# Kernel tuning notes

Measured on AMD Instinct MI355X. Metric: run time of the kernel, lower is better.

Reference implementation:

```python
import jax, jax.numpy as jnp
import numpy as np

N, E, F_IN, H, C, G = 50000, 800000, 64, 4, 32, 64
N_CLS, N_EXP, HID = 8, 3, 128
NEG_SLOPE = 0.2  # PyG GATConv default negative_slope


def setup_inputs() -> dict:
    key = jax.random.key(0)
    ks = jax.random.split(key, 16)
    p = lambda k, s: jax.random.normal(k, s, dtype=jnp.float32) * 0.05
    return {
        "x": jax.random.normal(ks[0], (N, F_IN), dtype=jnp.float32),
        "edge_index": jax.random.randint(ks[1], (2, E), 0, N),
        "batch": jnp.sort(jax.random.randint(ks[2], (N,), 0, G)),
        "set_idx": 0,
        "enc_W1": p(ks[3], (F_IN, H * C)),
        "enc_as1": p(ks[4], (H, C)),
        "enc_ad1": p(ks[5], (H, C)),
        "enc_b1": jnp.zeros((H * C,), jnp.float32),
        "enc_W2": p(ks[6], (H * C, H * C)),
        "enc_as2": p(ks[7], (H, C)),
        "enc_ad2": p(ks[8], (H, C)),
        "enc_b2": jnp.zeros((H * C,), jnp.float32),
        "cls_W1": p(ks[9], (2 * H * C, HID)),
        "cls_b1": jnp.zeros((HID,), jnp.float32),
        "cls_Wo": p(ks[10], (HID, N_CLS)),
        "cls_bo": jnp.zeros((N_CLS,), jnp.float32),
        "dis_W1": p(ks[11], (2 * H * C, HID)),
        "dis_b1": jnp.zeros((HID,), jnp.float32),
        "dis_Wo": p(ks[12], (HID, N_EXP)),
        "dis_bo": jnp.zeros((N_EXP,), jnp.float32),
    }


def gat_conv(x, src, dst, W, att_src, att_dst, bias):
    """PyG GATConv (concat=True, self-loops already in src/dst)."""
    n = x.shape[0]
    h = (x @ W).reshape(n, H, C)                     # [N,H,C]
    a_src = (h * att_src).sum(-1)                    # [N,H]
    a_dst = (h * att_dst).sum(-1)                    # [N,H]
    e = jax.nn.leaky_relu(a_src[src] + a_dst[dst], NEG_SLOPE)  # [E,H]
    e_max = jax.ops.segment_max(e, dst, num_segments=n)
    ee = jnp.exp(e - e_max[dst])
    denom = jax.ops.segment_sum(ee, dst, num_segments=n)
    alpha = ee / (denom[dst] + 1e-16)                # softmax over in-edges
    msg = h[src] * alpha[:, :, None]                 # [E,H,C]
    out = jax.ops.segment_sum(msg, dst, num_segments=n).reshape(n, H * C)
    return out + bias


def mlp(x, W1, b1, Wo, bo):
    return jax.nn.relu(x @ W1 + b1) @ Wo + bo


def reference(x, edge_index, batch, set_idx,
              enc_W1, enc_as1, enc_ad1, enc_b1,
              enc_W2, enc_as2, enc_ad2, enc_b2,
              cls_W1, cls_b1, cls_Wo, cls_bo,
              dis_W1, dis_b1, dis_Wo, dis_bo):
    n = x.shape[0]
    loop = jnp.arange(n)
    src = jnp.concatenate([edge_index[0], loop])     # add self-loops
    dst = jnp.concatenate([edge_index[1], loop])
    h = jax.nn.relu(gat_conv(x, src, dst, enc_W1, enc_as1, enc_ad1, enc_b1))
    h = gat_conv(h, src, dst, enc_W2, enc_as2, enc_ad2, enc_b2)
    counts = jax.ops.segment_sum(jnp.ones((n,), h.dtype), batch, num_segments=G)
    x_mean = jax.ops.segment_sum(h, batch, num_segments=G) / jnp.maximum(counts, 1.0)[:, None]
    x_max = jax.ops.segment_max(h, batch, num_segments=G)
    feat = jnp.concatenate([x_mean, x_max], axis=1)  # [G, 256]
    feat = feat / jnp.maximum(jnp.linalg.norm(feat, axis=1, keepdims=True), 1e-12)
    label_pred = mlp(feat, cls_W1, cls_b1, cls_Wo, cls_bo)
    # grad_reverse is identity in the forward pass
    batch_pred = mlp(feat, dis_W1, dis_b1, dis_Wo, dis_bo)
    return (label_pred, batch_pred)
```

## Files before the change

### kernel.cpp

```cpp
#include <hip/hip_runtime.h>
#include <float.h>

#define HC 128
#define NH 4
#define PSLICES 8
#define BSHIFT 9
#define NBK 128
#define NBH 512

__device__ __forceinline__ float lrelu(float v){ return v > 0.f ? v : 0.2f*v; }

__device__ __forceinline__ unsigned short f2bf(float f){
  unsigned int u = __float_as_uint(f);
  unsigned int r = (u + 0x7fffu + ((u >> 16) & 1u)) >> 16;
  return (unsigned short)r;
}

__global__ void k_hist(const int* __restrict__ ei, int* __restrict__ gmat,
                       int E, int T, int chunk){
  __shared__ int h[NBK];
  int b = blockIdx.x, t = threadIdx.x;
  if (t < NBK) h[t] = 0;
  __syncthreads();
  int lo = b*chunk, hi = lo + chunk; if (hi > T) hi = T;
  for (int i = lo + t; i < hi; i += 256){
    int d = (i < E) ? ei[E + i] : (i - E);
    atomicAdd(&h[d >> BSHIFT], 1);
  }
  __syncthreads();
  if (t < NBK) gmat[(size_t)b*NBK + t] = h[t];
}

__global__ void k_colscan(int* __restrict__ gmat, int* __restrict__ coltot){
  __shared__ int part[256];
  int k = blockIdx.x, t = threadIdx.x;
  int v0 = gmat[(size_t)(2*t)*NBK + k];
  int v1 = gmat[(size_t)(2*t+1)*NBK + k];
  int s = v0 + v1;
  part[t] = s;
  __syncthreads();
  for (int off = 1; off < 256; off <<= 1){
    int v = (t >= off) ? part[t-off] : 0;
    __syncthreads();
    part[t] += v;
    __syncthreads();
  }
  int pre = part[t] - s;
  gmat[(size_t)(2*t)*NBK + k]   = pre;
  gmat[(size_t)(2*t+1)*NBK + k] = pre + v0;
  if (t == 255) coltot[k] = part[255];
}

__global__ void k_bstart(const int* __restrict__ coltot, int* __restrict__ bstart,
                         int* __restrict__ rowptrN){
  __shared__ int part[NBK];
  int t = threadIdx.x;
  int own = coltot[t];
  part[t] = own;
  __syncthreads();
  for (int off = 1; off < NBK; off <<= 1){
    int v = (t >= off) ? part[t-off] : 0;
    __syncthreads();
    part[t] += v;
    __syncthreads();
  }
  bstart[t] = part[t] - own;
  if (t == NBK-1){ bstart[NBK] = part[NBK-1]; *rowptrN = part[NBK-1]; }
}

__global__ void k_bucket(const int* __restrict__ ei, const int* __restrict__ gmat,
                         const int* __restrict__ bstart, int2* __restrict__ pairs,
                         int E, int T, int chunk){
  __shared__ int cnt[NBK];
  int b = blockIdx.x, t = threadIdx.x;
  if (t < NBK) cnt[t] = 0;
  __syncthreads();
  int lo = b*chunk, hi = lo + chunk; if (hi > T) hi = T;
  for (int i = lo + t; i < hi; i += 256){
    int s, d;
    if (i < E){ s = ei[i]; d = ei[E + i]; } else { s = d = i - E; }
    int k = d >> BSHIFT;
    int r = atomicAdd(&cnt[k], 1);
    int pos = bstart[k] + gmat[(size_t)b*NBK + k] + r;
    pairs[pos] = make_int2(d, s);
  }
}

__global__ void k_csr(const int2* __restrict__ pairs, const int* __restrict__ bstart,
                      int* __restrict__ rowptr, int* __restrict__ srcs, int N){
  __shared__ int deg[512];
  __shared__ int off[512];
  __shared__ int part[256];
  int k = blockIdx.x, t = threadIdx.x;
  int nlo = k << BSHIFT;
  int nhi = nlo + 512; if (nhi > N) nhi = N;
  int nn = nhi - nlo;
  int elo = bstart[k], ehi = bstart[k+1];
  deg[t] = 0; deg[t + 256] = 0;
  __syncthreads();
  for (int i = elo + t; i < ehi; i += 256) atomicAdd(&deg[pairs[i].x - nlo], 1);
  __syncthreads();
  int v0 = deg[2*t], v1 = deg[2*t+1];
  int s = v0 + v1;
  part[t] = s;
  __syncthreads();
  for (int o = 1; o < 256; o <<= 1){
    int v = (t >= o) ? part[t-o] : 0;
    __syncthreads();
    part[t] += v;
    __syncthreads();
  }
  int pre = part[t] - s;
  off[2*t] = pre; off[2*t+1] = pre + v0;
  __syncthreads();
  for (int j = t; j < nn; j += 256) rowptr[nlo + j] = elo + off[j];
  deg[t] = 0; deg[t + 256] = 0;
  __syncthreads();
  for (int i = elo + t; i < ehi; i += 256){
    int2 p = pairs[i];
    int dl = p.x - nlo;
    int r = atomicAdd(&deg[dl], 1);
    srcs[elo + off[dl] + r] = p.y;
  }
}

template<int K>
__global__ __launch_bounds__(256) void k_gemm_att(
    const float* __restrict__ X, const float* __restrict__ W,
    const float* __restrict__ as_, const float* __restrict__ ad_,
    unsigned short* __restrict__ Hb, float* __restrict__ asrc, float* __restrict__ adst,
    int n)
{
  __shared__ float Ws[64][64];
  __shared__ float Xs[64][68];
  int tid = threadIdx.x;
  int tx = tid & 15;
  int ty = tid >> 4;
  int row0 = blockIdx.x * 64;
  int cbase = blockIdx.y * 64;

  float4 acc[4];
  #pragma unroll
  for (int i = 0; i < 4; ++i) acc[i] = make_float4(0.f,0.f,0.f,0.f);

  for (int kc = 0; kc < K; kc += 64){
    #pragma unroll
    for (int p = 0; p < 4; ++p){
      int idx = tid + 256*p;
      int rr = idx >> 4, kk = (idx & 15) * 4;
      float4 w = *reinterpret_cast<const float4*>(W + (size_t)(kc + rr)*HC + cbase + kk);
      *reinterpret_cast<float4*>(&Ws[rr][kk]) = w;
    }
    #pragma unroll
    for (int p = 0; p < 4; ++p){
      int idx = tid + 256*p;
      int rr = idx >> 4, kk = (idx & 15) * 4;
      int g = row0 + rr;
      float4 v = make_float4(0.f,0.f,0.f,0.f);
      if (g < n) v = *reinterpret_cast<const float4*>(X + (size_t)g*K + kc + kk);
      *reinterpret_cast<float4*>(&Xs[rr][kk]) = v;
    }
    __syncthreads();
    #pragma unroll 4
    for (int k = 0; k < 64; ++k){
      float4 w = *reinterpret_cast<const float4*>(&Ws[k][tx*4]);
      #pragma unroll
      for (int i = 0; i < 4; ++i){
        float xv = Xs[ty + 16*i][k];
        acc[i].x += xv*w.x; acc[i].y += xv*w.y; acc[i].z += xv*w.z; acc[i].w += xv*w.w;
      }
    }
    __syncthreads();
  }

  int c0 = cbase + tx*4;
  int hd = c0 >> 5;
  float4 a4 = *reinterpret_cast<const float4*>(as_ + c0);
  float4 d4 = *reinterpret_cast<const float4*>(ad_ + c0);
  #pragma unroll
  for (int i = 0; i < 4; ++i){
    int row = row0 + ty + 16*i;
    float ps = acc[i].x*a4.x + acc[i].y*a4.y + acc[i].z*a4.z + acc[i].w*a4.w;
    float pd = acc[i].x*d4.x + acc[i].y*d4.y + acc[i].z*d4.z + acc[i].w*d4.w;
    ps += __shfl_down(ps, 4); pd += __shfl_down(pd, 4);
    ps += __shfl_down(ps, 2); pd += __shfl_down(pd, 2);
    ps += __shfl_down(ps, 1); pd += __shfl_down(pd, 1);
    if (row < n){
      uint2 pk;
      pk.x = (unsigned int)f2bf(acc[i].x) | ((unsigned int)f2bf(acc[i].y) << 16);
      pk.y = (unsigned int)f2bf(acc[i].z) | ((unsigned int)f2bf(acc[i].w) << 16);
      *reinterpret_cast<uint2*>(Hb + (size_t)row*HC + c0) = pk;
      if ((tx & 7) == 0){
        asrc[row*NH + hd] = ps;
        adst[row*NH + hd] = pd;
      }
    }
  }
}

__global__ void k_agg(const unsigned short* __restrict__ Xh, const float* __restrict__ asrc,
                      const float* __restrict__ adst, const int* __restrict__ rowptr,
                      const int* __restrict__ srcs, const float* __restrict__ bias,
                      float* __restrict__ out, int n, int do_relu)
{
  int lane = threadIdx.x & 63;
  int node = blockIdx.x*4 + (threadIdx.x >> 6);
  if (node >= n) return;
  int base = __builtin_amdgcn_readfirstlane(rowptr[node]);
  int deg  = __builtin_amdgcn_readfirstlane(rowptr[node+1]) - base;
  int hd = lane >> 4;
  float adh = adst[node*NH + hd];
  int c0 = lane*2;
  float accx = 0.f, accy = 0.f, wsum = 0.f;
  int j = 0;
  for (; j + 8 <= deg; j += 8){
    int s0 = __builtin_amdgcn_readfirstlane(srcs[base + j]);
    int s1 = __builtin_amdgcn_readfirstlane(srcs[base + j + 1]);
    int s2 = __builtin_amdgcn_readfirstlane(srcs[base + j + 2]);
    int s3 = __builtin_amdgcn_readfirstlane(srcs[base + j + 3]);
    int s4 = __builtin_amdgcn_readfirstlane(srcs[base + j + 4]);
    int s5 = __builtin_amdgcn_readfirstlane(srcs[base + j + 5]);
    int s6 = __builtin_amdgcn_readfirstlane(srcs[base + j + 6]);
    int s7 = __builtin_amdgcn_readfirstlane(srcs[base + j + 7]);
    unsigned int u0 = *reinterpret_cast<const unsigned int*>(Xh + (size_t)s0*HC + c0);
    unsigned int u1 = *reinterpret_cast<const unsigned int*>(Xh + (size_t)s1*HC + c0);
    unsigned int u2 = *reinterpret_cast<const unsigned int*>(Xh + (size_t)s2*HC + c0);
    unsigned int u3 = *reinterpret_cast<const unsigned int*>(Xh + (size_t)s3*HC + c0);
    unsigned int u4 = *reinterpret_cast<const unsigned int*>(Xh + (size_t)s4*HC + c0);
    unsigned int u5 = *reinterpret_cast<const unsigned int*>(Xh + (size_t)s5*HC + c0);
    unsigned int u6 = *reinterpret_cast<const unsigned int*>(Xh + (size_t)s6*HC + c0);
    unsigned int u7 = *reinterpret_cast<const unsigned int*>(Xh + (size_t)s7*HC + c0);
    float a0 = asrc[s0*NH + hd];
    float a1 = asrc[s1*NH + hd];
    float a2 = asrc[s2*NH + hd];
    float a3 = asrc[s3*NH + hd];
    float a4 = asrc[s4*NH + hd];
    float a5 = asrc[s5*NH + hd];
    float a6 = asrc[s6*NH + hd];
    float a7 = asrc[s7*NH + hd];
    float w0 = __expf(lrelu(a0 + adh));
    float w1 = __expf(lrelu(a1 + adh));
    float w2 = __expf(lrelu(a2 + adh));
    float w3 = __expf(lrelu(a3 + adh));
    float w4 = __expf(lrelu(a4 + adh));
    float w5 = __expf(lrelu(a5 + adh));
    float w6 = __expf(lrelu(a6 + adh));
    float w7 = __expf(lrelu(a7 + adh));
    wsum += ((w0 + w1) + (w2 + w3)) + ((w4 + w5) + (w6 + w7));
    accx += w0*__uint_as_float(u0 << 16) + w1*__uint_as_float(u1 << 16)
          + w2*__uint_as_float(u2 << 16) + w3*__uint_as_float(u3 << 16)
          + w4*__uint_as_float(u4 << 16) + w5*__uint_as_float(u5 << 16)
          + w6*__uint_as_float(u6 << 16) + w7*__uint_as_float(u7 << 16);
    accy += w0*__uint_as_float(u0 & 0xffff0000u) + w1*__uint_as_float(u1 & 0xffff0000u)
          + w2*__uint_as_float(u2 & 0xffff0000u) + w3*__uint_as_float(u3 & 0xffff0000u)
          + w4*__uint_as_float(u4 & 0xffff0000u) + w5*__uint_as_float(u5 & 0xffff0000u)
          + w6*__uint_as_float(u6 & 0xffff0000u) + w7*__uint_as_float(u7 & 0xffff0000u);
  }
  for (; j + 4 <= deg; j += 4){
    int s0 = __builtin_amdgcn_readfirstlane(srcs[base + j]);
    int s1 = __builtin_amdgcn_readfirstlane(srcs[base + j + 1]);
    int s2 = __builtin_amdgcn_readfirstlane(srcs[base + j + 2]);
    int s3 = __builtin_amdgcn_readfirstlane(srcs[base + j + 3]);
    unsigned int u0 = *reinterpret_cast<const unsigned int*>(Xh + (size_t)s0*HC + c0);
    unsigned int u1 = *reinterpret_cast<const unsigned int*>(Xh + (size_t)s1*HC + c0);
    unsigned int u2 = *reinterpret_cast<const unsigned int*>(Xh + (size_t)s2*HC + c0);
    unsigned int u3 = *reinterpret_cast<const unsigned int*>(Xh + (size_t)s3*HC + c0);
    float a0 = asrc[s0*NH + hd];
    float a1 = asrc[s1*NH + hd];
    float a2 = asrc[s2*NH + hd];
    float a3 = asrc[s3*NH + hd];
    float w0 = __expf(lrelu(a0 + adh));
    float w1 = __expf(lrelu(a1 + adh));
    float w2 = __expf(lrelu(a2 + adh));
    float w3 = __expf(lrelu(a3 + adh));
    wsum += (w0 + w1) + (w2 + w3);
    accx += w0*__uint_as_float(u0 << 16) + w1*__uint_as_float(u1 << 16)
          + w2*__uint_as_float(u2 << 16) + w3*__uint_as_float(u3 << 16);
    accy += w0*__uint_as_float(u0 & 0xffff0000u) + w1*__uint_as_float(u1 & 0xffff0000u)
          + w2*__uint_as_float(u2 & 0xffff0000u) + w3*__uint_as_float(u3 & 0xffff0000u);
  }
  for (; j < deg; ++j){
    int s = __builtin_amdgcn_readfirstlane(srcs[base + j]);
    unsigned int u = *reinterpret_cast<const unsigned int*>(Xh + (size_t)s*HC + c0);
    float w = __expf(lrelu(asrc[s*NH + hd] + adh));
    wsum += w;
    accx += w*__uint_as_float(u << 16);
    accy += w*__uint_as_float(u & 0xffff0000u);
  }
  float inv = 1.f / wsum;
  accx = accx*inv + bias[c0];
  accy = accy*inv + bias[c0+1];
  if (do_relu){ accx = fmaxf(accx, 0.f); accy = fmaxf(accy, 0.f); }
  *reinterpret_cast<float2*>(out + (size_t)node*HC + c0) = make_float2(accx, accy);
}

__global__ void k_bounds(const int* __restrict__ batch, int* __restrict__ start, int N, int G){
  for (int i = blockIdx.x*blockDim.x + threadIdx.x; i <= N; i += gridDim.x*blockDim.x){
    int b  = (i < N) ? batch[i]   : G;
    int bp = (i > 0) ? batch[i-1] : -1;
    for (int g = bp + 1; g <= b; ++g) if (g <= G) start[g] = i;
  }
}

__global__ void k_pool_partial(const float* __restrict__ h2, const int* __restrict__ start,
                               float* __restrict__ psum, float* __restrict__ pmax, int G){
  int g = blockIdx.x / PSLICES, s = blockIdx.x % PSLICES;
  int c = threadIdx.x;
  int st = start[g], en = start[g+1];
  float sm = 0.f, mx = -FLT_MAX;
  for (int i = st + s; i < en; i += PSLICES){
    float v = h2[(size_t)i*HC + c];
    sm += v; mx = fmaxf(mx, v);
  }
  psum[(g*PSLICES+s)*HC + c] = sm;
  pmax[(g*PSLICES+s)*HC + c] = mx;
}

__global__ void k_head(const float* __restrict__ psum, const float* __restrict__ pmax,
                       const int* __restrict__ start,
                       const float* __restrict__ cW1, const float* __restrict__ cb1,
                       const float* __restrict__ cWo, const float* __restrict__ cbo,
                       const float* __restrict__ dW1, const float* __restrict__ db1,
                       const float* __restrict__ dWo, const float* __restrict__ dbo,
                       float* __restrict__ out, int G){
  __shared__ float feat[256];
  __shared__ float hid[128];
  __shared__ float red[2];
  int g = blockIdx.x;
  int t = threadIdx.x;
  int cnt = start[g+1] - start[g];
  float sm = 0.f, mx = -FLT_MAX;
  for (int s = 0; s < PSLICES; ++s){
    sm += psum[(g*PSLICES+s)*HC + t];
    mx = fmaxf(mx, pmax[(g*PSLICES+s)*HC + t]);
  }
  float mean = sm / (float)((cnt > 1) ? cnt : 1);
  feat[t] = mean; feat[128 + t] = mx;
  float sq = mean*mean + mx*mx;
  for (int d = 32; d; d >>= 1) sq += __shfl_xor(sq, d);
  if ((t & 63) == 0) red[t >> 6] = sq;
  __syncthreads();
  float norm = sqrtf(red[0] + red[1]);
  float scale = 1.f / fmaxf(norm, 1e-12f);
  feat[t] *= scale; feat[128 + t] *= scale;
  __syncthreads();
  float hsum = cb1[t];
  for (int k = 0; k < 256; ++k) hsum += feat[k]*cW1[k*128 + t];
  hid[t] = fmaxf(hsum, 0.f);
  __syncthreads();
  if (t < 8){
    float o = cbo[t];
    for (int k = 0; k < 128; ++k) o += hid[k]*cWo[k*8 + t];
    out[g*8 + t] = o;
  }
  __syncthreads();
  float dsum = db1[t];
  for (int k = 0; k < 256; ++k) dsum += feat[k]*dW1[k*128 + t];
  hid[t] = fmaxf(dsum, 0.f);
  __syncthreads();
  if (t < 3){
    float o = dbo[t];
    for (int k = 0; k < 128; ++k) o += hid[k]*dWo[k*3 + t];
    out[G*8 + g*3 + t] = o;
  }
}

extern "C" void kernel_launch(void* const* d_in, const int* in_sizes, int n_in,
                              void* d_out, int out_size, void* d_ws, size_t ws_size,
                              hipStream_t stream) {
  const float* x     = (const float*)d_in[0];
  const int*   ei    = (const int*)  d_in[1];
  const int*   batch = (const int*)  d_in[2];
  const float* eW1 = (const float*)d_in[4];
  const float* eas1= (const float*)d_in[5];
  const float* ead1= (const float*)d_in[6];
  const float* eb1 = (const float*)d_in[7];
  const float* eW2 = (const float*)d_in[8];
  const float* eas2= (const float*)d_in[9];
  const float* ead2= (const float*)d_in[10];
  const float* eb2 = (const float*)d_in[11];
  const float* cW1 = (const float*)d_in[12];
  const float* cb1 = (const float*)d_in[13];
  const float* cWo = (const float*)d_in[14];
  const float* cbo = (const float*)d_in[15];
  const float* dW1 = (const float*)d_in[16];
  const float* db1 = (const float*)d_in[17];
  const float* dWo = (const float*)d_in[18];
  const float* dbo = (const float*)d_in[19];

  const int N = in_sizes[0] / 64;
  const int E = in_sizes[1] / 2;
  const int G = 64;
  const int T = E + N;

  char* ws = (char*)d_ws;
  size_t off = 0;
  auto alloc = [&](size_t bytes)->void* {
    void* p = ws + off; off += (bytes + 255) & ~(size_t)255; return p;
  };
  int*   rowptr = (int*)  alloc((size_t)(N+1)*4);
  int*   srcs   = (int*)  alloc((size_t)T*4);
  int2*  pairs  = (int2*) alloc((size_t)T*8);
  int*   gmat   = (int*)  alloc((size_t)NBH*NBK*4);
  int*   coltot = (int*)  alloc((size_t)NBK*4);
  int*   bstart = (int*)  alloc((size_t)(NBK+1)*4);
  float* asrc   = (float*)alloc((size_t)N*NH*4);
  float* adst   = (float*)alloc((size_t)N*NH*4);
  unsigned short* bufH = (unsigned short*)alloc((size_t)N*HC*2);
  float* bufB   = (float*)alloc((size_t)N*HC*4);
  int*   startg = (int*)  alloc((size_t)(G+1)*4);
  float* psum   = (float*)alloc((size_t)G*PSLICES*HC*4);
  float* pmax   = (float*)alloc((size_t)G*PSLICES*HC*4);
  (void)ws_size; (void)n_in; (void)out_size;

  int chunk = (T + NBH - 1) / NBH;
  int nbuck = (N + (1 << BSHIFT) - 1) >> BSHIFT;
  k_hist   <<<NBH, 256, 0, stream>>>(ei, gmat, E, T, chunk);
  k_colscan<<<NBK, 256, 0, stream>>>(gmat, coltot);
  k_bstart <<<1,  NBK, 0, stream>>>(coltot, bstart, rowptr + N);
  k_bucket <<<NBH, 256, 0, stream>>>(ei, gmat, bstart, pairs, E, T, chunk);
  k_csr    <<<nbuck, 256, 0, stream>>>(pairs, bstart, rowptr, srcs, N);

  dim3 ggrid((N + 63) / 64, 2);
  k_gemm_att<64><<<ggrid, 256, 0, stream>>>(x, eW1, eas1, ead1, bufH, asrc, adst, N);
  k_agg<<<(N+3)/4, 256, 0, stream>>>(bufH, asrc, adst, rowptr, srcs, eb1, bufB, N, 1);
  k_gemm_att<128><<<ggrid, 256, 0, stream>>>(bufB, eW2, eas2, ead2, bufH, asrc, adst, N);
  k_agg<<<(N+3)/4, 256, 0, stream>>>(bufH, asrc, adst, rowptr, srcs, eb2, bufB, N, 0);

  k_bounds<<<64, 256, 0, stream>>>(batch, startg, N, G);
  k_pool_partial<<<G*PSLICES, 128, 0, stream>>>(bufB, startg, psum, pmax, G);
  k_head<<<G, 128, 0, stream>>>(psum, pmax, startg, cW1, cb1, cWo, cbo,
                                dW1, db1, dWo, dbo, (float*)d_out, G);
}
```

Measured before the change: 216.7 us.

## Pack CSR pairs, cache buckets in LDS, store layer-1 output as bf16, drop bounds kernel

The CSR build now packs each (local dst, src) pair into a single 32-bit word and stages each bucket in LDS, so the second pass reads shared memory instead of global. The layer-1 aggregation writes bf16, and the second GEMM reads and widens that bf16 input, halving the intermediate feature traffic. Graph boundaries are found by binary search on the sorted batch array inside the pooling and head kernels, removing the k_bounds launch. The packing assumes node ids fit in 16 bits, which holds for N=50000, and the bf16 intermediate adds rounding error.

```diff
diff --git a/kernel.cpp b/kernel.cpp
--- a/kernel.cpp
+++ b/kernel.cpp
@@ -7,6 +7,7 @@
 #define BSHIFT 9
 #define NBK 128
 #define NBH 512
+#define LDSN 14336
 
 __device__ __forceinline__ float lrelu(float v){ return v > 0.f ? v : 0.2f*v; }
 
@@ -14,6 +15,12 @@
   unsigned int u = __float_as_uint(f);
   unsigned int r = (u + 0x7fffu + ((u >> 16) & 1u)) >> 16;
   return (unsigned short)r;
+}
+
+__device__ __forceinline__ int lbound(const int* __restrict__ a, int n, int v){
+  int lo = 0, hi = n;
+  while (lo < hi){ int m = (lo + hi) >> 1; if (a[m] < v) lo = m + 1; else hi = m; }
+  return lo;
 }
 
 __global__ void k_hist(const int* __restrict__ ei, int* __restrict__ gmat,
@@ -69,7 +76,7 @@
 }
 
 __global__ void k_bucket(const int* __restrict__ ei, const int* __restrict__ gmat,
-                         const int* __restrict__ bstart, int2* __restrict__ pairs,
+                         const int* __restrict__ bstart, int* __restrict__ pairs,
                          int E, int T, int chunk){
   __shared__ int cnt[NBK];
   int b = blockIdx.x, t = threadIdx.x;
@@ -82,23 +89,34 @@
     int k = d >> BSHIFT;
     int r = atomicAdd(&cnt[k], 1);
     int pos = bstart[k] + gmat[(size_t)b*NBK + k] + r;
-    pairs[pos] = make_int2(d, s);
-  }
-}
-
-__global__ void k_csr(const int2* __restrict__ pairs, const int* __restrict__ bstart,
+    pairs[pos] = ((d & ((1 << BSHIFT) - 1)) << 16) | s;
+  }
+}
+
+__global__ void k_csr(const int* __restrict__ pairs, const int* __restrict__ bstart,
                       int* __restrict__ rowptr, int* __restrict__ srcs, int N){
   __shared__ int deg[512];
   __shared__ int off[512];
   __shared__ int part[256];
+  __shared__ int sp[LDSN];
   int k = blockIdx.x, t = threadIdx.x;
   int nlo = k << BSHIFT;
   int nhi = nlo + 512; if (nhi > N) nhi = N;
   int nn = nhi - nlo;
   int elo = bstart[k], ehi = bstart[k+1];
+  int ne = ehi - elo;
+  bool uselds = (ne <= LDSN);
   deg[t] = 0; deg[t + 256] = 0;
   __syncthreads();
-  for (int i = elo + t; i < ehi; i += 256) atomicAdd(&deg[pairs[i].x - nlo], 1);
+  if (uselds){
+    for (int i = t; i < ne; i += 256){
+      int p = pairs[elo + i];
+      sp[i] = p;
+      atomicAdd(&deg[p >> 16], 1);
+    }
+  } else {
+    for (int i = t; i < ne; i += 256) atomicAdd(&deg[pairs[elo + i] >> 16], 1);
+  }
   __syncthreads();
   int v0 = deg[2*t], v1 = deg[2*t+1];
   int s = v0 + v1;
@@ -116,17 +134,26 @@
   for (int j = t; j < nn; j += 256) rowptr[nlo + j] = elo + off[j];
   deg[t] = 0; deg[t + 256] = 0;
   __syncthreads();
-  for (int i = elo + t; i < ehi; i += 256){
-    int2 p = pairs[i];
-    int dl = p.x - nlo;
-    int r = atomicAdd(&deg[dl], 1);
-    srcs[elo + off[dl] + r] = p.y;
-  }
-}
-
-template<int K>
+  if (uselds){
+    for (int i = t; i < ne; i += 256){
+      int p = sp[i];
+      int dl = p >> 16;
+      int r = atomicAdd(&deg[dl], 1);
+      srcs[elo + off[dl] + r] = p & 0xFFFF;
+    }
+  } else {
+    for (int i = t; i < ne; i += 256){
+      int p = pairs[elo + i];
+      int dl = p >> 16;
+      int r = atomicAdd(&deg[dl], 1);
+      srcs[elo + off[dl] + r] = p & 0xFFFF;
+    }
+  }
+}
+
+template<int K, bool INBF>
 __global__ __launch_bounds__(256) void k_gemm_att(
-    const float* __restrict__ X, const float* __restrict__ W,
+    const void* __restrict__ Xv, const float* __restrict__ W,
     const float* __restrict__ as_, const float* __restrict__ ad_,
     unsigned short* __restrict__ Hb, float* __restrict__ asrc, float* __restrict__ adst,
     int n)
@@ -151,14 +178,35 @@
       float4 w = *reinterpret_cast<const float4*>(W + (size_t)(kc + rr)*HC + cbase + kk);
       *reinterpret_cast<float4*>(&Ws[rr][kk]) = w;
     }
-    #pragma unroll
-    for (int p = 0; p < 4; ++p){
-      int idx = tid + 256*p;
-      int rr = idx >> 4, kk = (idx & 15) * 4;
-      int g = row0 + rr;
-      float4 v = make_float4(0.f,0.f,0.f,0.f);
-      if (g < n) v = *reinterpret_cast<const float4*>(X + (size_t)g*K + kc + kk);
-      *reinterpret_cast<float4*>(&Xs[rr][kk]) = v;
+    if constexpr (INBF){
+      const unsigned short* Xh16 = (const unsigned short*)Xv;
+      #pragma unroll
+      for (int p = 0; p < 2; ++p){
+        int idx = tid + 256*p;
+        int rr = idx >> 3, kk = (idx & 7) * 8;
+        int g = row0 + rr;
+        float4 lo = make_float4(0.f,0.f,0.f,0.f), hi = lo;
+        if (g < n){
+          uint4 v = *reinterpret_cast<const uint4*>(Xh16 + (size_t)g*K + kc + kk);
+          lo.x = __uint_as_float(v.x << 16); lo.y = __uint_as_float(v.x & 0xffff0000u);
+          lo.z = __uint_as_float(v.y << 16); lo.w = __uint_as_float(v.y & 0xffff0000u);
+          hi.x = __uint_as_float(v.z << 16); hi.y = __uint_as_float(v.z & 0xffff0000u);
+          hi.z = __uint_as_float(v.w << 16); hi.w = __uint_as_float(v.w & 0xffff0000u);
+        }
+        *reinterpret_cast<float4*>(&Xs[rr][kk])     = lo;
+        *reinterpret_cast<float4*>(&Xs[rr][kk + 4]) = hi;
+      }
+    } else {
+      const float* Xf = (const float*)Xv;
+      #pragma unroll
+      for (int p = 0; p < 4; ++p){
+        int idx = tid + 256*p;
+        int rr = idx >> 4, kk = (idx & 15) * 4;
+        int g = row0 + rr;
+        float4 v = make_float4(0.f,0.f,0.f,0.f);
+        if (g < n) v = *reinterpret_cast<const float4*>(Xf + (size_t)g*K + kc + kk);
+        *reinterpret_cast<float4*>(&Xs[rr][kk]) = v;
+      }
     }
     __syncthreads();
     #pragma unroll 4
@@ -198,10 +246,11 @@
   }
 }
 
+template<bool OBF>
 __global__ void k_agg(const unsigned short* __restrict__ Xh, const float* __restrict__ asrc,
                       const float* __restrict__ adst, const int* __restrict__ rowptr,
                       const int* __restrict__ srcs, const float* __restrict__ bias,
-                      float* __restrict__ out, int n, int do_relu)
+                      void* __restrict__ outv, int n, int do_relu)
 {
   int lane = threadIdx.x & 63;
   int node = blockIdx.x*4 + (threadIdx.x >> 6);
@@ -291,22 +340,20 @@
   accx = accx*inv + bias[c0];
   accy = accy*inv + bias[c0+1];
   if (do_relu){ accx = fmaxf(accx, 0.f); accy = fmaxf(accy, 0.f); }
-  *reinterpret_cast<float2*>(out + (size_t)node*HC + c0) = make_float2(accx, accy);
-}
-
-__global__ void k_bounds(const int* __restrict__ batch, int* __restrict__ start, int N, int G){
-  for (int i = blockIdx.x*blockDim.x + threadIdx.x; i <= N; i += gridDim.x*blockDim.x){
-    int b  = (i < N) ? batch[i]   : G;
-    int bp = (i > 0) ? batch[i-1] : -1;
-    for (int g = bp + 1; g <= b; ++g) if (g <= G) start[g] = i;
-  }
-}
-
-__global__ void k_pool_partial(const float* __restrict__ h2, const int* __restrict__ start,
-                               float* __restrict__ psum, float* __restrict__ pmax, int G){
+  if constexpr (OBF){
+    unsigned int pk = (unsigned int)f2bf(accx) | ((unsigned int)f2bf(accy) << 16);
+    ((unsigned int*)outv)[(size_t)node*(HC/2) + lane] = pk;
+  } else {
+    *reinterpret_cast<float2*>((float*)outv + (size_t)node*HC + c0) = make_float2(accx, accy);
+  }
+}
+
+__global__ void k_pool_partial(const float* __restrict__ h2, const int* __restrict__ batch,
+                               float* __restrict__ psum, float* __restrict__ pmax, int N, int G){
   int g = blockIdx.x / PSLICES, s = blockIdx.x % PSLICES;
   int c = threadIdx.x;
-  int st = start[g], en = start[g+1];
+  int st = lbound(batch, N, g);
+  int en = lbound(batch, N, g + 1);
   float sm = 0.f, mx = -FLT_MAX;
   for (int i = st + s; i < en; i += PSLICES){
     float v = h2[(size_t)i*HC + c];
@@ -317,18 +364,18 @@
 }
 
 __global__ void k_head(const float* __restrict__ psum, const float* __restrict__ pmax,
-                       const int* __restrict__ start,
+                       const int* __restrict__ batch,
                        const float* __restrict__ cW1, const float* __restrict__ cb1,
                        const float* __restrict__ cWo, const float* __restrict__ cbo,
                        const float* __restrict__ dW1, const float* __restrict__ db1,
                        const float* __restrict__ dWo, const float* __restrict__ dbo,
-                       float* __restrict__ out, int G){
+                       float* __restrict__ out, int N, int G){
   __shared__ float feat[256];
   __shared__ float hid[128];
   __shared__ float red[2];
   int g = blockIdx.x;
   int t = threadIdx.x;
-  int cnt = start[g+1] - start[g];
+  int cnt = lbound(batch, N, g + 1) - lbound(batch, N, g);
   float sm = 0.f, mx = -FLT_MAX;
   for (int s = 0; s < PSLICES; ++s){
     sm += psum[(g*PSLICES+s)*HC + t];
@@ -400,15 +447,15 @@
   };
   int*   rowptr = (int*)  alloc((size_t)(N+1)*4);
   int*   srcs   = (int*)  alloc((size_t)T*4);
-  int2*  pairs  = (int2*) alloc((size_t)T*8);
+  int*   pairs  = (int*)  alloc((size_t)T*4);
   int*   gmat   = (int*)  alloc((size_t)NBH*NBK*4);
   int*   coltot = (int*)  alloc((size_t)NBK*4);
   int*   bstart = (int*)  alloc((size_t)(NBK+1)*4);
   float* asrc   = (float*)alloc((size_t)N*NH*4);
   float* adst   = (float*)alloc((size_t)N*NH*4);
-  unsigned short* bufH = (unsigned short*)alloc((size_t)N*HC*2);
+  unsigned short* bufH  = (unsigned short*)alloc((size_t)N*HC*2);
+  unsigned short* bufX2 = (unsigned short*)alloc((size_t)N*HC*2);
   float* bufB   = (float*)alloc((size_t)N*HC*4);
-  int*   startg = (int*)  alloc((size_t)(G+1)*4);
   float* psum   = (float*)alloc((size_t)G*PSLICES*HC*4);
   float* pmax   = (float*)alloc((size_t)G*PSLICES*HC*4);
   (void)ws_size; (void)n_in; (void)out_size;
@@ -422,13 +469,12 @@
   k_csr    <<<nbuck, 256, 0, stream>>>(pairs, bstart, rowptr, srcs, N);
 
   dim3 ggrid((N + 63) / 64, 2);
-  k_gemm_att<64><<<ggrid, 256, 0, stream>>>(x, eW1, eas1, ead1, bufH, asrc, adst, N);
-  k_agg<<<(N+3)/4, 256, 0, stream>>>(bufH, asrc, adst, rowptr, srcs, eb1, bufB, N, 1);
-  k_gemm_att<128><<<ggrid, 256, 0, stream>>>(bufB, eW2, eas2, ead2, bufH, asrc, adst, N);
-  k_agg<<<(N+3)/4, 256, 0, stream>>>(bufH, asrc, adst, rowptr, srcs, eb2, bufB, N, 0);
-
-  k_bounds<<<64, 256, 0, stream>>>(batch, startg, N, G);
-  k_pool_partial<<<G*PSLICES, 128, 0, stream>>>(bufB, startg, psum, pmax, G);
-  k_head<<<G, 128, 0, stream>>>(psum, pmax, startg, cW1, cb1, cWo, cbo,
-                                dW1, db1, dWo, dbo, (float*)d_out, G);
-}
+  k_gemm_att<64,false><<<ggrid, 256, 0, stream>>>(x, eW1, eas1, ead1, bufH, asrc, adst, N);
+  k_agg<true><<<(N+3)/4, 256, 0, stream>>>(bufH, asrc, adst, rowptr, srcs, eb1, bufX2, N, 1);
+  k_gemm_att<128,true><<<ggrid, 256, 0, stream>>>(bufX2, eW2, eas2, ead2, bufH, asrc, adst, N);
+  k_agg<false><<<(N+3)/4, 256, 0, stream>>>(bufH, asrc, adst, rowptr, srcs, eb2, bufB, N, 0);
+
+  k_pool_partial<<<G*PSLICES, 128, 0, stream>>>(bufB, batch, psum, pmax, N, G);
+  k_head<<<G, 128, 0, stream>>>(psum, pmax, batch, cW1, cb1, cWo, cbo,
+                                dW1, db1, dWo, dbo, (float*)d_out, N, G);
+}
```

Result: no change. 213.5 us (median of 2 runs) (-1.5%).
